# Kernel optimization log

Hardware: AMD Instinct MI355X
Metric: run time of the kernel (lower is better)

The kernel has to match this reference:

```python
import jax, jax.numpy as jnp
import numpy as np

B, T, D = 4, 2048, 2048
H = 16
HO = D // H  # head_out = 128


def setup_inputs() -> dict:
    key = jax.random.key(0)
    ks = jax.random.split(key, 6)
    x = jax.random.normal(ks[0], (B, T, D), dtype=jnp.float32)
    scale = 0.02
    Wq = jax.random.normal(ks[1], (D, D), dtype=jnp.float32) * scale
    Wk = jax.random.normal(ks[2], (D, D), dtype=jnp.float32) * scale
    Wv = jax.random.normal(ks[3], (D, D), dtype=jnp.float32) * scale
    Wp = jax.random.normal(ks[4], (D, D), dtype=jnp.float32) * scale
    bp = jnp.zeros((D,), dtype=jnp.float32)
    return {"x": x, "Wq": Wq, "Wk": Wk, "Wv": Wv, "Wp": Wp, "bp": bp}


def reference(x, Wq, Wk, Wv, Wp, bp):
    b, t, _ = x.shape
    # QKV projections (weights stored [d_in, d_out])
    q = x @ Wq
    k = x @ Wk
    v = x @ Wv
    split = lambda a: a.reshape(b, t, H, HO).transpose(0, 2, 1, 3)  # [b,H,T,ho]
    qh, kh, vh = split(q), split(k), split(v)
    # Feature attention: contract over tokens -> [b,H,ho,ho]
    scores = jnp.einsum('bhtf,bhtg->bhfg', qh, kh) / jnp.sqrt(jnp.float32(HO))
    weights = jax.nn.softmax(scores, axis=-1)  # dropout p=0.0 (identity)
    # feature_alibi: [1/T, 1/(T-1), ..., 1], broadcast over batch/head/feature
    feat_alibi = (1.0 / jnp.arange(t, 0, -1, dtype=jnp.float32)).reshape(1, 1, t, 1)
    vh = vh + feat_alibi
    # (weights @ v^T)^T : ctx[b,h,t,f] = sum_g weights[b,h,f,g] * v[b,h,t,g]
    ctx = jnp.einsum('bhfg,bhtg->bhtf', weights, vh)
    ctx = ctx.transpose(0, 2, 1, 3).reshape(b, t, H * HO)  # [b,T,d_out]
    return ctx @ Wp + bp
```

## Files before the change

### kernel.cpp

```cpp
#include <hip/hip_runtime.h>
#include <hip/hip_bf16.h>


#define Tt 2048
#define Dd 2048
#define Mm 8192

typedef __attribute__((ext_vector_type(4))) float f32x4;
typedef __attribute__((ext_vector_type(8))) short s16x8;
static_assert(sizeof(s16x8) == 16, "frag size");

typedef const __attribute__((address_space(1))) void* gptr_t;
typedef __attribute__((address_space(3))) void* lptr_t;

__device__ __forceinline__ float bf2f(ushort u) {
    union { unsigned int i; float f; } c; c.i = ((unsigned int)u) << 16; return c.f;
}
__device__ __forceinline__ ushort f2bf(float f) {
    union { float f; unsigned int i; } c; c.f = f;
    return (ushort)((c.i + 0x7FFFu + ((c.i >> 16) & 1u)) >> 16);
}
__device__ __forceinline__ void gload16(const void* g, void* l) {
    __builtin_amdgcn_global_load_lds((gptr_t)g, (lptr_t)l, 16, 0, 0);
}
__device__ __forceinline__ s16x8 ldfrag(const char* p) { return *(const s16x8*)p; }

#define MFMA_BF16(d, a, b) \
    d = __builtin_amdgcn_mfma_f32_16x16x32_bf16((a), (b), (d), 0, 0, 0)


__global__ __launch_bounds__(256) void convxT_kernel(const float* __restrict__ x,
        ushort* __restrict__ xb, ushort* __restrict__ xT) {
    __shared__ float tile[64][65];
    const int b = blockIdx.z;
    const int t0 = blockIdx.y * 64, d0 = blockIdx.x * 64;
    const int r4 = threadIdx.x >> 6, c = threadIdx.x & 63;
#pragma unroll
    for (int i = 0; i < 16; i++) {
        const int row = i * 4 + r4;
        const size_t g = ((size_t)b * Tt + t0 + row) * Dd + d0 + c;
        const float val = x[g];
        xb[g] = f2bf(val);
        tile[row][c] = val;
    }
    __syncthreads();
#pragma unroll
    for (int i = 0; i < 16; i++) {
        const int row = i * 4 + r4;
        xT[(size_t)b * ((size_t)Dd * Tt) + (size_t)(d0 + row) * Tt + t0 + c] =
            f2bf(tile[c][row]);
    }
}


__global__ __launch_bounds__(256) void transw_kernel(const float* __restrict__ W0,
        const float* __restrict__ W1, const float* __restrict__ W2,
        const float* __restrict__ W3, ushort* __restrict__ Wt,
        float* __restrict__ S) {
    __shared__ float tile[64][65];
    const int z = blockIdx.z;
    const float* W = (z == 0) ? W0 : (z == 1) ? W1 : (z == 2) ? W2 : W3;
    ushort* dst = Wt + (size_t)z * ((size_t)Dd * Dd);
    const int n0 = blockIdx.x * 64, k0 = blockIdx.y * 64;
    const int r4 = threadIdx.x >> 6, c = threadIdx.x & 63;
#pragma unroll
    for (int i = 0; i < 16; i++) {
        const int row = i * 4 + r4;
        tile[row][c] = W[(size_t)(k0 + row) * Dd + n0 + c];
    }
    __syncthreads();
#pragma unroll
    for (int i = 0; i < 16; i++) {
        const int row = i * 4 + r4;
        dst[(size_t)(n0 + row) * Dd + k0 + c] = f2bf(tile[c][row]);
    }
    if (z == 3) {
        float partial = 0.f;
#pragma unroll
        for (int i = 0; i < 16; i++) partial += tile[r4 * 16 + i][c];
        atomicAdd(&S[n0 + c], partial);
    }
}


__device__ __forceinline__ void stage_half(char* ldsRegion, const ushort* gRegion,
                                           int ld, int half, int tid) {
#pragma unroll
    for (int j = 0; j < 2; j++) {
        const int Pb = half * 16384 + j * 8192 + (tid >> 6) * 1024;
        const int P = Pb + (tid & 63) * 16;
        const int row = P >> 7;
        const int colb = (P ^ ((row & 7) << 4)) & 127;
        gload16(gRegion + (size_t)row * ld + (colb >> 1), ldsRegion + Pb);
    }
}

template <int MODE>
__global__ __launch_bounds__(512, 2) void gemm256_kernel(
        const ushort* __restrict__ A, const ushort* __restrict__ Bt,
        void* __restrict__ Cv, const float* __restrict__ bias,
        const float* __restrict__ S,
        int Kdim, int lda, int ldb, int ldc,
        size_t astride, size_t bstride, size_t cstride) {
    extern __shared__ char lds[];

    const int tid = threadIdx.x;
    const int lane = tid & 63;
    const int w = tid >> 6;
    const int wr = w >> 2, wc = w & 3;
    const int fr = lane & 15, fq = lane >> 4;

    const int bid = blockIdx.x;
    const int cpx = (int)gridDim.x >> 3;
    const int wg = (bid & 7) * cpx + (bid >> 3);
    const int m0 = (wg >> 3) * 256;
    const int n0 = (wg & 7) * 256;

    const ushort* Ag = A + (size_t)blockIdx.z * astride + (size_t)m0 * lda;
    const ushort* Bg = Bt + (size_t)blockIdx.z * bstride + (size_t)n0 * ldb;
    const int NT = Kdim >> 6;

    const int aoff = wr * 16384 + fr * 128;
    const int boff = wc * 8192 + fr * 128;
    const int xo = (fr & 7) << 4;
    const int cp0 = (fq * 16) ^ xo;
    const int cp1 = (64 + fq * 16) ^ xo;

    char* buf0 = lds;
    char* buf1 = lds + 65536;
    const char* Ab0 = buf0 + aoff;
    const char* Bb0 = buf0 + 32768 + boff;
    const char* Ab1 = buf1 + aoff;
    const char* Bb1 = buf1 + 32768 + boff;

    f32x4 acc[8][4];
#pragma unroll
    for (int i = 0; i < 8; i++)
#pragma unroll
        for (int j = 0; j < 4; j++) acc[i][j] = {0.f, 0.f, 0.f, 0.f};

    s16x8 afX[4][2], afY[4][2], bf01[2][2], bf23[2][2];

    {
        stage_half(buf0,         Ag, lda, 0, tid);
        stage_half(buf0,         Ag, lda, 1, tid);
        stage_half(buf0 + 32768, Bg, ldb, 0, tid);
        stage_half(buf0 + 32768, Bg, ldb, 1, tid);
        stage_half(buf1,         Ag + 64, lda, 0, tid);
        stage_half(buf1 + 32768, Bg + 64, ldb, 0, tid);
        stage_half(buf1 + 32768, Bg + 64, ldb, 1, tid);
        asm volatile("s_waitcnt vmcnt(6)" ::: "memory");
        __builtin_amdgcn_sched_barrier(0);
        __builtin_amdgcn_s_barrier();
    }

    const int NI = NT >> 1;
    for (int j = 0; j < NI; ++j) {
        const int e = 2 * j;
        const bool sE2 = (e + 2 < NT);
        const bool sO2 = (e + 3 < NT);
        const ushort* AgO  = Ag + (size_t)(e + 1) * 64;
        const ushort* AgE2 = Ag + (size_t)(e + 2) * 64;
        const ushort* BgE2 = Bg + (size_t)(e + 2) * 64;
        const ushort* AgO2 = Ag + (size_t)(e + 3) * 64;
        const ushort* BgO2 = Bg + (size_t)(e + 3) * 64;

        stage_half(buf1, AgO, lda, 1, tid);
#pragma unroll
        for (int m = 0; m < 4; m++) {
            afX[m][0] = ldfrag(Ab0 + m * 2048 + cp0);
            afX[m][1] = ldfrag(Ab0 + m * 2048 + cp1);
        }
#pragma unroll
        for (int n = 0; n < 2; n++) {
            bf01[n][0] = ldfrag(Bb0 + n * 2048 + cp0);
            bf01[n][1] = ldfrag(Bb0 + n * 2048 + cp1);
        }
        __builtin_amdgcn_s_barrier();
        __builtin_amdgcn_s_setprio(1);
#pragma unroll
        for (int k = 0; k < 2; k++)
#pragma unroll
            for (int m = 0; m < 4; m++)
#pragma unroll
                for (int n = 0; n < 2; n++) MFMA_BF16(acc[m][n], afX[m][k], bf01[n][k]);
        __builtin_amdgcn_s_setprio(0);
        __builtin_amdgcn_s_barrier();

#pragma unroll
        for (int n = 0; n < 2; n++) {
            bf23[n][0] = ldfrag(Bb0 + (n + 2) * 2048 + cp0);
            bf23[n][1] = ldfrag(Bb0 + (n + 2) * 2048 + cp1);
        }
        __builtin_amdgcn_s_barrier();
        __builtin_amdgcn_s_setprio(1);
#pragma unroll
        for (int k = 0; k < 2; k++)
#pragma unroll
            for (int m = 0; m < 4; m++)
#pragma unroll
                for (int n = 0; n < 2; n++) MFMA_BF16(acc[m][n + 2], afX[m][k], bf23[n][k]);
        __builtin_amdgcn_s_setprio(0);
        __builtin_amdgcn_s_barrier();

        if (sE2) stage_half(buf0 + 32768, BgE2, ldb, 0, tid);
#pragma unroll
        for (int m = 0; m < 4; m++) {
            afY[m][0] = ldfrag(Ab0 + (m + 4) * 2048 + cp0);
            afY[m][1] = ldfrag(Ab0 + (m + 4) * 2048 + cp1);
        }
        __builtin_amdgcn_s_barrier();
        __builtin_amdgcn_s_setprio(1);
#pragma unroll
        for (int k = 0; k < 2; k++)
#pragma unroll
            for (int m = 0; m < 4; m++)
#pragma unroll
                for (int n = 0; n < 2; n++) MFMA_BF16(acc[m + 4][n], afY[m][k], bf01[n][k]);
        __builtin_amdgcn_s_setprio(0);
        __builtin_amdgcn_s_barrier();

        if (sE2) stage_half(buf0 + 32768, BgE2, ldb, 1, tid);
        __builtin_amdgcn_s_setprio(1);
#pragma unroll
        for (int k = 0; k < 2; k++)
#pragma unroll
            for (int m = 0; m < 4; m++)
#pragma unroll
                for (int n = 0; n < 2; n++) MFMA_BF16(acc[m + 4][n + 2], afY[m][k], bf23[n][k]);
        __builtin_amdgcn_s_setprio(0);
        if (sE2) asm volatile("s_waitcnt vmcnt(4)" ::: "memory");
        else     asm volatile("s_waitcnt vmcnt(0)" ::: "memory");
        __builtin_amdgcn_sched_barrier(0);
        __builtin_amdgcn_s_barrier();

        if (sE2) stage_half(buf0, AgE2, lda, 0, tid);
#pragma unroll
        for (int m = 0; m < 4; m++) {
            afX[m][0] = ldfrag(Ab1 + m * 2048 + cp0);
            afX[m][1] = ldfrag(Ab1 + m * 2048 + cp1);
        }
#pragma unroll
        for (int n = 0; n < 2; n++) {
            bf01[n][0] = ldfrag(Bb1 + n * 2048 + cp0);
            bf01[n][1] = ldfrag(Bb1 + n * 2048 + cp1);
        }
        __builtin_amdgcn_s_barrier();
        __builtin_amdgcn_s_setprio(1);
#pragma unroll
        for (int k = 0; k < 2; k++)
#pragma unroll
            for (int m = 0; m < 4; m++)
#pragma unroll
                for (int n = 0; n < 2; n++) MFMA_BF16(acc[m][n], afX[m][k], bf01[n][k]);
        __builtin_amdgcn_s_setprio(0);
        __builtin_amdgcn_s_barrier();

        if (sE2) stage_half(buf0, AgE2, lda, 1, tid);
#pragma unroll
        for (int n = 0; n < 2; n++) {
            bf23[n][0] = ldfrag(Bb1 + (n + 2) * 2048 + cp0);
            bf23[n][1] = ldfrag(Bb1 + (n + 2) * 2048 + cp1);
        }
        __builtin_amdgcn_s_barrier();
        __builtin_amdgcn_s_setprio(1);
#pragma unroll
        for (int k = 0; k < 2; k++)
#pragma unroll
            for (int m = 0; m < 4; m++)
#pragma unroll
                for (int n = 0; n < 2; n++) MFMA_BF16(acc[m][n + 2], afX[m][k], bf23[n][k]);
        __builtin_amdgcn_s_setprio(0);
        __builtin_amdgcn_s_barrier();

        if (sO2) stage_half(buf1 + 32768, BgO2, ldb, 0, tid);
#pragma unroll
        for (int m = 0; m < 4; m++) {
            afY[m][0] = ldfrag(Ab1 + (m + 4) * 2048 + cp0);
            afY[m][1] = ldfrag(Ab1 + (m + 4) * 2048 + cp1);
        }
        __builtin_amdgcn_s_barrier();
        __builtin_amdgcn_s_setprio(1);
#pragma unroll
        for (int k = 0; k < 2; k++)
#pragma unroll
            for (int m = 0; m < 4; m++)
#pragma unroll
                for (int n = 0; n < 2; n++) MFMA_BF16(acc[m + 4][n], afY[m][k], bf01[n][k]);
        __builtin_amdgcn_s_setprio(0);
        __builtin_amdgcn_s_barrier();

        if (sO2) {
            stage_half(buf1 + 32768, BgO2, ldb, 1, tid);
            stage_half(buf1, AgO2, lda, 0, tid);
        }
        __builtin_amdgcn_s_setprio(1);
#pragma unroll
        for (int k = 0; k < 2; k++)
#pragma unroll
            for (int m = 0; m < 4; m++)
#pragma unroll
                for (int n = 0; n < 2; n++) MFMA_BF16(acc[m + 4][n + 2], afY[m][k], bf23[n][k]);
        __builtin_amdgcn_s_setprio(0);
        if (sO2)      asm volatile("s_waitcnt vmcnt(6)" ::: "memory");
        else if (sE2) asm volatile("s_waitcnt vmcnt(4)" ::: "memory");
        else          asm volatile("s_waitcnt vmcnt(0)" ::: "memory");
        __builtin_amdgcn_sched_barrier(0);
        __builtin_amdgcn_s_barrier();
    }

    if (MODE == 2) {
        float* C = (float*)Cv + (size_t)blockIdx.z * cstride;
#pragma unroll
        for (int mi = 0; mi < 8; mi++)
#pragma unroll
            for (int ni = 0; ni < 4; ni++)
#pragma unroll
                for (int r = 0; r < 4; r++) {
                    const int row = m0 + wr * 128 + mi * 16 + fq * 4 + r;
                    const int col = n0 + wc * 64 + ni * 16 + fr;
                    const float alibi = 1.0f / (float)(Tt - row);
                    C[(size_t)row * ldc + col] =
                        acc[mi][ni][r] + alibi * S[col] + bias[col];
                }
    } else {
        ushort* C = (ushort*)Cv + (size_t)blockIdx.z * cstride;
#pragma unroll
        for (int mi = 0; mi < 8; mi++)
#pragma unroll
            for (int ni = 0; ni < 4; ni++)
#pragma unroll
                for (int r = 0; r < 4; r++) {
                    const int row = m0 + wr * 128 + mi * 16 + fq * 4 + r;
                    const int col = n0 + wc * 64 + ni * 16 + fr;
                    C[(size_t)row * ldc + col] = f2bf(acc[mi][ni][r]);
                }
    }
}


template <int MODE>
__global__ __launch_bounds__(256, 2) void gemm_kernel(
        const ushort* __restrict__ A, const ushort* __restrict__ Bt,
        void* __restrict__ Cv,
        int Kdim, int lda, int ldb, int ldc) {
    __shared__ ushort lsA[128 * 32];
    __shared__ ushort lsB[128 * 32];

    const int tid = threadIdx.x;
    const int w = tid >> 6, lane = tid & 63;
    const int m0 = blockIdx.y * 128;
    const int n0 = blockIdx.x * 128;

    const ushort* Ab = A;
    const ushort* Bb = Bt;
    size_t coff = 0;
    if (MODE == 3) {
        const int z = blockIdx.z, s = z >> 6, bh = z & 63;
        const int b = bh >> 4, h = bh & 15;
        Ab += (size_t)h * 128 * Dd + (size_t)s * 256;
        Bb += (size_t)b * ((size_t)Dd * Dd) + (size_t)h * 128 * Dd + (size_t)s * 256;
        coff = (size_t)s * (64 * 16384) + (size_t)bh * 16384;
    }
    if (MODE == 4) {
        const int z = blockIdx.z, b = z >> 4, h = z & 15;
        Ab += (size_t)h * 128;
        Bb += (size_t)z * 16384;
        coff = (size_t)b * ((size_t)Dd * Dd) + (size_t)h * 128;
    }

    const int sr = lane >> 2;
    const int sc = (lane & 3) * 8;
    const int c0 = w, c1 = w + 4;
    const int rA0 = c0 * 16 + sr, rA1 = c1 * 16 + sr;

    const int fr = lane & 15, fq = lane >> 4;
    const int wr = (w >> 1) * 64, wc = (w & 1) * 64;

    f32x4 acc[4][4];
#pragma unroll
    for (int i = 0; i < 4; i++)
#pragma unroll
        for (int j = 0; j < 4; j++) acc[i][j] = {0.f, 0.f, 0.f, 0.f};

    for (int kt = 0; kt < Kdim; kt += 32) {
        gload16(Ab + (size_t)(m0 + rA0) * lda + kt + sc, lsA + c0 * 512);
        gload16(Ab + (size_t)(m0 + rA1) * lda + kt + sc, lsA + c1 * 512);
        gload16(Bb + (size_t)(n0 + rA0) * ldb + kt + sc, lsB + c0 * 512);
        gload16(Bb + (size_t)(n0 + rA1) * ldb + kt + sc, lsB + c1 * 512);
        __syncthreads();

        s16x8 afrag[4], bfrag[4];
#pragma unroll
        for (int i = 0; i < 4; i++)
            afrag[i] = *(const s16x8*)(lsA + (wr + i * 16 + fr) * 32 + fq * 8);
#pragma unroll
        for (int j = 0; j < 4; j++)
            bfrag[j] = *(const s16x8*)(lsB + (wc + j * 16 + fr) * 32 + fq * 8);
#pragma unroll
        for (int i = 0; i < 4; i++)
#pragma unroll
            for (int j = 0; j < 4; j++)
                MFMA_BF16(acc[i][j], afrag[i], bfrag[j]);
        __syncthreads();
    }

    if (MODE == 3) {
        float* C = (float*)Cv + coff;
#pragma unroll
        for (int i = 0; i < 4; i++)
#pragma unroll
            for (int j = 0; j < 4; j++)
#pragma unroll
                for (int r = 0; r < 4; r++) {
                    const int row = m0 + wr + i * 16 + fq * 4 + r;
                    const int col = n0 + wc + j * 16 + fr;
                    C[(size_t)row * ldc + col] = acc[i][j][r];
                }
    } else {
        ushort* C = (ushort*)Cv + coff;
#pragma unroll
        for (int i = 0; i < 4; i++)
#pragma unroll
            for (int j = 0; j < 4; j++)
#pragma unroll
                for (int r = 0; r < 4; r++) {
                    const int row = m0 + wr + i * 16 + fq * 4 + r;
                    const int col = n0 + wc + j * 16 + fr;
                    C[(size_t)row * ldc + col] = f2bf(acc[i][j][r]);
                }
    }
}


__global__ __launch_bounds__(256) void softmax_kernel(const float* __restrict__ part,
                                                      ushort* __restrict__ wtsT) {
    const int tid = threadIdx.x;
    const int wv = tid >> 6, lane = tid & 63;
    const int row = blockIdx.x * 4 + wv;
    const float* p = part + (size_t)row * 128 + lane * 2;
    float v0 = 0.f, v1 = 0.f;
#pragma unroll
    for (int s = 0; s < 8; s++) {
        const float2 t = *(const float2*)(p + (size_t)s * 1048576);
        v0 += t.x; v1 += t.y;
    }
    const float sc = 0.088388347648318447f;
    v0 *= sc; v1 *= sc;
    float m = fmaxf(v0, v1);
#pragma unroll
    for (int off = 32; off > 0; off >>= 1) m = fmaxf(m, __shfl_xor(m, off));
    const float e0 = __expf(v0 - m), e1 = __expf(v1 - m);
    float smv = e0 + e1;
#pragma unroll
    for (int off = 32; off > 0; off >>= 1) smv += __shfl_xor(smv, off);
    const float inv = 1.0f / smv;
    const int bh = row >> 7, f = row & 127;
    ushort* o = wtsT + (size_t)bh * 16384 + (size_t)(lane * 2) * 128 + f;
    o[0]   = f2bf(e0 * inv);
    o[128] = f2bf(e1 * inv);
}


extern "C" void kernel_launch(void* const* d_in, const int* in_sizes, int n_in,
                              void* d_out, int out_size, void* d_ws, size_t ws_size,
                              hipStream_t stream) {
    const float* x  = (const float*)d_in[0];
    const float* Wq = (const float*)d_in[1];
    const float* Wk = (const float*)d_in[2];
    const float* Wv = (const float*)d_in[3];
    const float* Wp = (const float*)d_in[4];
    const float* bp = (const float*)d_in[5];
    float* out = (float*)d_out;
    char* ws = (char*)d_ws;

    ushort* xb   = (ushort*)(ws);
    ushort* xT   = (ushort*)(ws + (32ull << 20));
    ushort* Wt   = (ushort*)(ws + (64ull << 20));
    ushort* G    = (ushort*)(ws + (96ull << 20));
    ushort* Hb   = (ushort*)(ws + (128ull << 20));
    ushort* v    = (ushort*)(ws + (160ull << 20));
    float*  part = (float*) (ws + (96ull << 20));
    ushort* wtsT = (ushort*)(ws + (192ull << 20));
    float*  S    = (float*) (ws + (194ull << 20));
    ushort* Mt   = xT;

    const size_t WSZ = (size_t)Dd * Dd;
    const size_t TD  = (size_t)Tt * Dd;

    static_cast<void>(hipFuncSetAttribute((const void*)gemm256_kernel<0>,
        hipFuncAttributeMaxDynamicSharedMemorySize, 131072));
    static_cast<void>(hipFuncSetAttribute((const void*)gemm256_kernel<2>,
        hipFuncAttributeMaxDynamicSharedMemorySize, 131072));

    static_cast<void>(hipMemsetAsync(S, 0, Dd * sizeof(float), stream));
    convxT_kernel<<<dim3(32, 32, 4), 256, 0, stream>>>(x, xb, xT);
    transw_kernel<<<dim3(32, 32, 4), 256, 0, stream>>>(Wq, Wk, Wv, Wp, Wt, S);

    gemm256_kernel<0><<<dim3(64, 1, 4), 512, 131072, stream>>>(
        xT, xT, G, nullptr, nullptr, 2048, 2048, 2048, 2048, WSZ, WSZ, WSZ);

    gemm256_kernel<0><<<dim3(64, 1, 4), 512, 131072, stream>>>(
        Wt + WSZ, G, Hb, nullptr, nullptr, 2048, 2048, 2048, 2048, 0, WSZ, WSZ);

    gemm256_kernel<0><<<dim3(256, 1, 1), 512, 131072, stream>>>(
        xb, Wt + 2 * WSZ, v, nullptr, nullptr, 2048, 2048, 2048, 2048, 0, 0, 0);

    gemm_kernel<3><<<dim3(1, 1, 512), 256, 0, stream>>>(
        Wt, Hb, part, 256, 2048, 2048, 128);

    softmax_kernel<<<2048, 256, 0, stream>>>(part, wtsT);

    gemm_kernel<4><<<dim3(1, 16, 64), 256, 0, stream>>>(
        Wt + 3 * WSZ, wtsT, Mt, 128, 2048, 128, 2048);

    gemm256_kernel<2><<<dim3(64, 1, 4), 512, 131072, stream>>>(
        v, Mt, out, bp, S, 2048, 2048, 2048, 2048, TD, WSZ, TD);
}
```

Before: 354.5 us.

## Exploit symmetry of Gram matrix: compute upper triangle tiles then mirror

The Gram matrix G = x^T x per batch is symmetric, so a new kernel computes only the 136 upper-triangular 128x128 tiles with a double-buffered LDS MFMA loop. A second kernel then copies those tiles into the lower triangle through an LDS transpose. This roughly halves the FLOPs of that GEMM but adds an extra launch, a read/write pass over half of G, and uses smaller 128-tile blocks that may be less efficient than the 256-tile kernel.

```diff
diff --git a/kernel.cpp b/kernel.cpp
--- a/kernel.cpp
+++ b/kernel.cpp
@@ -79,6 +79,143 @@
 #pragma unroll
         for (int i = 0; i < 16; i++) partial += tile[r4 * 16 + i][c];
         atomicAdd(&S[n0 + c], partial);
+    }
+}
+
+
+__device__ __forceinline__ void stage_tile(char* region, const ushort* g, int ld, int tid) {
+#pragma unroll
+    for (int j = 0; j < 4; j++) {
+        const int Pb = j * 4096 + (tid >> 6) * 1024;
+        const int P = Pb + (tid & 63) * 16;
+        const int row = P >> 7;
+        const int colb = (P ^ ((row & 7) << 4)) & 127;
+        gload16(g + (size_t)row * ld + (colb >> 1), region + Pb);
+    }
+}
+
+__global__ __launch_bounds__(256, 2) void gemmG_kernel(
+        const ushort* __restrict__ xT, ushort* __restrict__ G) {
+    extern __shared__ char lds[];
+
+    const int tid = threadIdx.x;
+    const int lane = tid & 63;
+    const int w = tid >> 6;
+    const int wr = w >> 1, wc = w & 1;
+    const int fr = lane & 15, fq = lane >> 4;
+
+    const int bid = blockIdx.x;
+    const int wg = (bid & 7) * 17 + (bid >> 3);
+    int I = 0, rem = wg;
+    while (rem >= 16 - I) { rem -= 16 - I; ++I; }
+    const int J = I + rem;
+    const int m0 = I * 128, n0 = J * 128;
+
+    const size_t bb = (size_t)blockIdx.z * ((size_t)Dd * Tt);
+    const ushort* Ag = xT + bb + (size_t)m0 * Tt;
+    const ushort* Bg = xT + bb + (size_t)n0 * Tt;
+    const int NT = Tt >> 6;
+
+    const int aoff = (wr * 64 + fr) * 128;
+    const int boff = (wc * 64 + fr) * 128;
+    const int xo = (fr & 7) << 4;
+    const int cp0 = (fq * 16) ^ xo;
+    const int cp1 = (64 + fq * 16) ^ xo;
+
+    f32x4 acc[4][4];
+#pragma unroll
+    for (int i = 0; i < 4; i++)
+#pragma unroll
+        for (int j = 0; j < 4; j++) acc[i][j] = {0.f, 0.f, 0.f, 0.f};
+
+    s16x8 af[4][2], bf[4][2];
+
+    stage_tile(lds,         Ag,      Tt, tid);
+    stage_tile(lds + 16384, Bg,      Tt, tid);
+    stage_tile(lds + 32768, Ag + 64, Tt, tid);
+    stage_tile(lds + 49152, Bg + 64, Tt, tid);
+    __builtin_amdgcn_sched_barrier(0);
+    asm volatile("s_waitcnt vmcnt(8)" ::: "memory");
+    __builtin_amdgcn_s_barrier();
+
+    for (int t = 0; t < NT; ++t) {
+        char* buf = lds + (t & 1) * 32768;
+        const char* Ab = buf + aoff;
+        const char* Bb = buf + 16384 + boff;
+
+#pragma unroll
+        for (int m = 0; m < 4; m++) {
+            af[m][0] = ldfrag(Ab + m * 2048 + cp0);
+            af[m][1] = ldfrag(Ab + m * 2048 + cp1);
+        }
+#pragma unroll
+        for (int n = 0; n < 4; n++) {
+            bf[n][0] = ldfrag(Bb + n * 2048 + cp0);
+            bf[n][1] = ldfrag(Bb + n * 2048 + cp1);
+        }
+        __builtin_amdgcn_sched_barrier(0);
+        asm volatile("s_waitcnt lgkmcnt(0)" ::: "memory");
+        __builtin_amdgcn_sched_barrier(0);
+        __builtin_amdgcn_s_setprio(1);
+#pragma unroll
+        for (int k = 0; k < 2; k++)
+#pragma unroll
+            for (int m = 0; m < 4; m++)
+#pragma unroll
+                for (int n = 0; n < 4; n++) MFMA_BF16(acc[m][n], af[m][k], bf[n][k]);
+        __builtin_amdgcn_s_setprio(0);
+        __builtin_amdgcn_s_barrier();
+
+        if (t + 2 < NT) {
+            stage_tile(buf,         Ag + (size_t)(t + 2) * 64, Tt, tid);
+            stage_tile(buf + 16384, Bg + (size_t)(t + 2) * 64, Tt, tid);
+        }
+        __builtin_amdgcn_sched_barrier(0);
+        if (t + 2 < NT) asm volatile("s_waitcnt vmcnt(8)" ::: "memory");
+        else            asm volatile("s_waitcnt vmcnt(0)" ::: "memory");
+        __builtin_amdgcn_s_barrier();
+    }
+
+    ushort* C = G + (size_t)blockIdx.z * ((size_t)Dd * Dd);
+#pragma unroll
+    for (int mi = 0; mi < 4; mi++)
+#pragma unroll
+        for (int ni = 0; ni < 4; ni++)
+#pragma unroll
+            for (int r = 0; r < 4; r++) {
+                const int row = m0 + wr * 64 + mi * 16 + fq * 4 + r;
+                const int col = n0 + wc * 64 + ni * 16 + fr;
+                C[(size_t)row * Dd + col] = f2bf(acc[mi][ni][r]);
+            }
+}
+
+
+__global__ __launch_bounds__(256) void symmG_kernel(ushort* __restrict__ G) {
+    __shared__ ushort t64[64][65];
+    const int bid = blockIdx.x;
+    const int wg = (bid & 7) * 15 + (bid >> 3);
+    int I = 0, rem = wg;
+    while (rem >= 15 - I) { rem -= 15 - I; ++I; }
+    const int J = I + 1 + rem;
+    ushort* Gb = G + (size_t)blockIdx.z * ((size_t)Dd * Dd);
+    const int r4 = threadIdx.x >> 6, c = threadIdx.x & 63;
+#pragma unroll
+    for (int sub = 0; sub < 4; ++sub) {
+        const int p = sub >> 1, q = sub & 1;
+        const ushort* src = Gb + (size_t)(I * 128 + q * 64) * Dd + J * 128 + p * 64;
+        ushort*       dst = Gb + (size_t)(J * 128 + p * 64) * Dd + I * 128 + q * 64;
+#pragma unroll
+        for (int i = 0; i < 16; i++) {
+            const int row = i * 4 + r4;
+            t64[row][c] = src[(size_t)row * Dd + c];
+        }
+        __syncthreads();
+#pragma unroll
+        for (int i = 0; i < 16; i++) {
+            const int row = i * 4 + r4;
+            dst[(size_t)row * Dd + c] = t64[c][row];
+        }
+        __syncthreads();
     }
 }
 
@@ -492,13 +629,15 @@
         hipFuncAttributeMaxDynamicSharedMemorySize, 131072));
     static_cast<void>(hipFuncSetAttribute((const void*)gemm256_kernel<2>,
         hipFuncAttributeMaxDynamicSharedMemorySize, 131072));
+    static_cast<void>(hipFuncSetAttribute((const void*)gemmG_kernel,
+        hipFuncAttributeMaxDynamicSharedMemorySize, 65536));
 
     static_cast<void>(hipMemsetAsync(S, 0, Dd * sizeof(float), stream));
     convxT_kernel<<<dim3(32, 32, 4), 256, 0, stream>>>(x, xb, xT);
     transw_kernel<<<dim3(32, 32, 4), 256, 0, stream>>>(Wq, Wk, Wv, Wp, Wt, S);
 
-    gemm256_kernel<0><<<dim3(64, 1, 4), 512, 131072, stream>>>(
-        xT, xT, G, nullptr, nullptr, 2048, 2048, 2048, 2048, WSZ, WSZ, WSZ);
+    gemmG_kernel<<<dim3(136, 1, 4), 256, 65536, stream>>>(xT, G);
+    symmG_kernel<<<dim3(120, 1, 4), 256, 0, stream>>>(G);
 
     gemm256_kernel<0><<<dim3(64, 1, 4), 512, 131072, stream>>>(
         Wt + WSZ, G, Hb, nullptr, nullptr, 2048, 2048, 2048, 2048, 0, WSZ, WSZ);
```

Measured after the change: 365.0 us. +3.0%, slower.
